# Kernel optimization log

Hardware: AMD Instinct MI355X
Metric: run time of the kernel (lower is better)

Reference implementation:

```python
import jax, jax.numpy as jnp
import numpy as np

K = 2  # kernel_size == stride, padding=0, dilation=1 -> non-overlapping 2x2x2 blocks


def setup_inputs() -> dict:
    key = jax.random.key(0)
    # (b, c, s, w, h) volumetric batch
    x = jax.random.normal(key, (8, 1, 64, 192, 192), dtype=jnp.float32)
    return {"x": x}


def _extract_blocks(x, k):
    # Faithful to extract_patches_3d with stride==kernel, padding=0, dilation=1:
    # the double unfold + permute + flat view yields rows ordered (b, c, do, ho, wo),
    # each row the flattened k*k*k patch.
    b, c, s, w, h = x.shape
    blk = x.reshape(b, c, s // k, k, w // k, k, h // k, k)
    blk = blk.transpose(0, 1, 2, 4, 6, 3, 5, 7)  # (b,c,do,ho,wo,k,k,k)
    return blk.reshape(-1, k * k * k)  # (N, k^3)


def reference(x):
    b, c, s, w, h = x.shape
    data = _extract_blocks(x, K)            # (N, 8)
    mean = jnp.mean(data, axis=0)           # (8,)
    centered = data - mean
    # torch.svd: data = U S V^T ; jax returns vh = V^T
    _, _, vh = jnp.linalg.svd(centered, full_matrices=False)
    pca_components = vh[:1].T               # (8, n_components=1)
    reduced = centered @ pca_components     # (N, 1)
    out = reduced.reshape(b, c, s // K, w // K, h // K)
    return out, mean, pca_components
```

## Files before the change

kernel.cpp:

```cpp
#include <hip/hip_runtime.h>

constexpr int NB     = 8 * 32 * 96 * 96;
constexpr int NQUAD  = NB / 4;
constexpr int NACC   = 44;
constexpr int GRID_A = 768;
constexpr int TPB    = 256;
constexpr int GRID_P = 768;

__global__ __launch_bounds__(TPB, 4)
void reduce_kernel(const float* __restrict__ x, float* __restrict__ partials) {
  float acc[NACC];
#pragma unroll
  for (int i = 0; i < NACC; ++i) acc[i] = 0.0f;

  int tid = blockIdx.x * TPB + threadIdx.x;
  const int stride = GRID_A * TPB;
  for (int q = tid; q < NQUAD; q += stride) {
    int hq = q % 24;
    int t1 = q / 24;
    int wo = t1 % 96;
    int t2 = t1 / 96;
    int so = t2 % 32;
    int b  = t2 / 32;
    const float* base = x + (((b * 64 + 2 * so) * 192 + 2 * wo) * 192 + 8 * hq);
    float4 a0 = *(const float4*)(base);
    float4 b0 = *(const float4*)(base + 4);
    float4 a1 = *(const float4*)(base + 192);
    float4 b1 = *(const float4*)(base + 196);
    float4 a2 = *(const float4*)(base + 192 * 192);
    float4 b2 = *(const float4*)(base + 192 * 192 + 4);
    float4 a3 = *(const float4*)(base + 192 * 192 + 192);
    float4 b3 = *(const float4*)(base + 192 * 192 + 196);
    float P[4][8] = {
      {a0.x, a0.y, a1.x, a1.y, a2.x, a2.y, a3.x, a3.y},
      {a0.z, a0.w, a1.z, a1.w, a2.z, a2.w, a3.z, a3.w},
      {b0.x, b0.y, b1.x, b1.y, b2.x, b2.y, b3.x, b3.y},
      {b0.z, b0.w, b1.z, b1.w, b2.z, b2.w, b3.z, b3.w}};
#pragma unroll
    for (int a = 0; a < 8; ++a)
      acc[a] += (P[0][a] + P[1][a]) + (P[2][a] + P[3][a]);
    int k = 8;
#pragma unroll
    for (int a = 0; a < 8; ++a)
#pragma unroll
      for (int c = a; c < 8; ++c) {
        float t = P[0][a] * P[0][c];
        t += P[1][a] * P[1][c];
        t += P[2][a] * P[2][c];
        t += P[3][a] * P[3][c];
        acc[k++] += t;
      }
  }

#pragma unroll
  for (int i = 0; i < NACC; ++i) {
    float v = acc[i];
    for (int off = 32; off >= 1; off >>= 1) v += __shfl_down(v, off, 64);
    acc[i] = v;
  }
  __shared__ float lds[4][NACC];
  int lane = threadIdx.x & 63;
  int wv   = threadIdx.x >> 6;
  if (lane == 0) {
#pragma unroll
    for (int i = 0; i < NACC; ++i) lds[wv][i] = acc[i];
  }
  __syncthreads();
  if (threadIdx.x < NACC) {
    float s = lds[0][threadIdx.x] + lds[1][threadIdx.x] +
              lds[2][threadIdx.x] + lds[3][threadIdx.x];
    partials[threadIdx.x * GRID_A + blockIdx.x] = s;
  }
}

__global__ __launch_bounds__(TPB)
void mid_reduce_kernel(const float* __restrict__ partials, double* __restrict__ sums_d) {
  int a = blockIdx.x;
  int t = threadIdx.x;
  const float* row = partials + a * GRID_A;
  double s = (double)row[t] + (double)row[t + 256] + (double)row[t + 512];
  for (int off = 32; off >= 1; off >>= 1) s += __shfl_down(s, off, 64);
  __shared__ double lds[4];
  if ((t & 63) == 0) lds[t >> 6] = s;
  __syncthreads();
  if (t == 0) sums_d[a] = lds[0] + lds[1] + lds[2] + lds[3];
}

__device__ __forceinline__ float rdlane(float x, int lane) {
  return __int_as_float(__builtin_amdgcn_readlane(__float_as_int(x), lane));
}

template <int P, int Q>
__device__ __forceinline__ void jrot(const float (&r)[8], float& ct, float& st) {
  float app = rdlane(r[P], P);
  float aqq = rdlane(r[Q], Q);
  float apq = rdlane(r[Q], P);
  float theta = (aqq - app) * 0.5f * __builtin_amdgcn_rcpf(apq);
  float root  = __builtin_amdgcn_sqrtf(theta * theta + 1.0f);
  float tmag  = __builtin_amdgcn_rcpf(fabsf(theta) + root);
  float tt    = copysignf(tmag, theta);
  float c     = __builtin_amdgcn_rsqf(tt * tt + 1.0f);
  float s     = tt * c;
  bool zero   = (apq == 0.0f);
  ct = zero ? 1.0f : c;
  st = zero ? 0.0f : s;
}

template <int P, int Q>
__device__ __forceinline__ void jcol(float (&r)[8], float (&v)[8], float c, float s) {
  float rp = r[P], rq = r[Q];
  r[P] = c * rp - s * rq;
  r[Q] = s * rp + c * rq;
  float vp = v[P], vq = v[Q];
  v[P] = c * vp - s * vq;
  v[Q] = s * vp + c * vq;
}

template <int P0,int Q0,int P1,int Q1,int P2,int Q2,int P3,int Q3>
__device__ __forceinline__ void jacobi_round(float (&r)[8], float (&v)[8], int i) {
  float c0,s0,c1,s1,c2,s2,c3,s3;
  jrot<P0,Q0>(r, c0, s0);
  jrot<P1,Q1>(r, c1, s1);
  jrot<P2,Q2>(r, c2, s2);
  jrot<P3,Q3>(r, c3, s3);
  jcol<P0,Q0>(r, v, c0, s0);
  jcol<P1,Q1>(r, v, c1, s1);
  jcol<P2,Q2>(r, v, c2, s2);
  jcol<P3,Q3>(r, v, c3, s3);
  float alpha = 1.0f, beta = 0.0f;
  int plane = i;
  if (i == P0) { alpha = c0; beta = -s0; plane = Q0; }
  if (i == Q0) { alpha = c0; beta =  s0; plane = P0; }
  if (i == P1) { alpha = c1; beta = -s1; plane = Q1; }
  if (i == Q1) { alpha = c1; beta =  s1; plane = P1; }
  if (i == P2) { alpha = c2; beta = -s2; plane = Q2; }
  if (i == Q2) { alpha = c2; beta =  s2; plane = P2; }
  if (i == P3) { alpha = c3; beta = -s3; plane = Q3; }
  if (i == Q3) { alpha = c3; beta =  s3; plane = P3; }
  float prow[8];
#pragma unroll
  for (int j = 0; j < 8; ++j) prow[j] = __shfl(r[j], plane, 64);
#pragma unroll
  for (int j = 0; j < 8; ++j) r[j] = alpha * r[j] + beta * prow[j];
}

__global__ __launch_bounds__(TPB, 4)
void project_solve_kernel(const float* __restrict__ x,
                          const double* __restrict__ sums_d,
                          float* __restrict__ out,
                          float* __restrict__ out_tail) {
  __shared__ double sums[NACC];
  __shared__ float s_res[9];
  int t = threadIdx.x;

  if (t < NACC) sums[t] = sums_d[t];
  __syncthreads();

  if (t < 64) {
    const int i = t & 7;
    const double invN = 1.0 / (double)NB;
    double mean[8];
#pragma unroll
    for (int j = 0; j < 8; ++j) mean[j] = sums[j] * invN;
    double mean_i = mean[0];
#pragma unroll
    for (int k = 1; k < 8; ++k) if (i == k) mean_i = mean[k];
    double rowd[8];
#pragma unroll
    for (int j = 0; j < 8; ++j) {
      int p = i < j ? i : j;
      int q = i < j ? j : i;
      int idx = 8 + p * 8 - (p * (p - 1)) / 2 + (q - p);
      rowd[j] = sums[idx] - (double)NB * mean_i * mean[j];
    }
    double tr = 0.0;
#pragma unroll
    for (int k = 0; k < 8; ++k) tr += __shfl(rowd[k], k, 64);
    double shift = tr * 0.125;

    float r[8], v[8];
#pragma unroll
    for (int j = 0; j < 8; ++j) {
      double d = rowd[j] - (j == i ? shift : 0.0);
      r[j] = (float)(d * (1.0 / 1536.0));
      v[j] = (j == i) ? 1.0f : 0.0f;
    }
#pragma unroll 1
    for (int sweep = 0; sweep < 6; ++sweep) {
      jacobi_round<7,0, 1,6, 2,5, 3,4>(r, v, i);
      jacobi_round<7,1, 2,0, 3,6, 4,5>(r, v, i);
      jacobi_round<7,2, 3,1, 4,0, 5,6>(r, v, i);
      jacobi_round<7,3, 4,2, 5,1, 6,0>(r, v, i);
      jacobi_round<7,4, 5,3, 6,2, 0,1>(r, v, i);
      jacobi_round<7,5, 6,4, 0,3, 1,2>(r, v, i);
      jacobi_round<7,6, 0,5, 1,4, 2,3>(r, v, i);
    }
    float diag[8];
#pragma unroll
    for (int k = 0; k < 8; ++k) diag[k] = rdlane(r[k], k);
    int best = 0; float bd = diag[0];
#pragma unroll
    for (int k = 1; k < 8; ++k) if (diag[k] > bd) { bd = diag[k]; best = k; }
    float vi = v[0];
#pragma unroll
    for (int k = 1; k < 8; ++k) if (best == k) vi = v[k];
    float vec[8];
#pragma unroll
    for (int k = 0; k < 8; ++k) vec[k] = rdlane(vi, k);
    float nrm2 = 0.0f;
#pragma unroll
    for (int k = 0; k < 8; ++k) nrm2 += vec[k] * vec[k];
    float inv = 1.0f / sqrtf(nrm2);
#pragma unroll
    for (int k = 0; k < 8; ++k) vec[k] *= inv;
    int m = 0; float am = fabsf(vec[0]);
#pragma unroll
    for (int k = 1; k < 8; ++k) { float aa = fabsf(vec[k]); if (aa > am) { am = aa; m = k; } }
    float vm = vec[0];
#pragma unroll
    for (int k = 1; k < 8; ++k) if (m == k) vm = vec[k];
    if (vm > 0.0f) {
#pragma unroll
      for (int k = 0; k < 8; ++k) vec[k] = -vec[k];
    }
    double c0d = 0.0;
#pragma unroll
    for (int k = 0; k < 8; ++k) c0d += mean[k] * (double)vec[k];
    float mi = (float)mean[0];
#pragma unroll
    for (int k = 1; k < 8; ++k) if (i == k) mi = (float)mean[k];
    float vl = vec[0];
#pragma unroll
    for (int k = 1; k < 8; ++k) if (i == k) vl = vec[k];

    if (t < 8) {
      s_res[t] = vl;
      if (blockIdx.x == 0) {
        out_tail[t]     = mi;
        out_tail[8 + t] = vl;
      }
    }
    if (t == 0) s_res[8] = (float)c0d;
  }
  __syncthreads();

  float w0 = s_res[0], w1 = s_res[1], w2 = s_res[2], w3 = s_res[3];
  float w4 = s_res[4], w5 = s_res[5], w6 = s_res[6], w7 = s_res[7];
  float c0 = s_res[8];
  float4* out4 = (float4*)out;
  const int stride = GRID_P * TPB;
  for (int q = blockIdx.x * TPB + t; q < NQUAD; q += stride) {
    int hq = q % 24;
    int t1 = q / 24;
    int wo = t1 % 96;
    int t2 = t1 / 96;
    int so = t2 % 32;
    int b  = t2 / 32;
    const float* base = x + (((b * 64 + 2 * so) * 192 + 2 * wo) * 192 + 8 * hq);
    float4 a0 = *(const float4*)(base);
    float4 b0 = *(const float4*)(base + 4);
    float4 a1 = *(const float4*)(base + 192);
    float4 b1 = *(const float4*)(base + 196);
    float4 a2 = *(const float4*)(base + 192 * 192);
    float4 b2 = *(const float4*)(base + 192 * 192 + 4);
    float4 a3 = *(const float4*)(base + 192 * 192 + 192);
    float4 b3 = *(const float4*)(base + 192 * 192 + 196);
    float o0 = a0.x * w0 + a0.y * w1 + a1.x * w2 + a1.y * w3
             + a2.x * w4 + a2.y * w5 + a3.x * w6 + a3.y * w7 - c0;
    float o1 = a0.z * w0 + a0.w * w1 + a1.z * w2 + a1.w * w3
             + a2.z * w4 + a2.w * w5 + a3.z * w6 + a3.w * w7 - c0;
    float o2 = b0.x * w0 + b0.y * w1 + b1.x * w2 + b1.y * w3
             + b2.x * w4 + b2.y * w5 + b3.x * w6 + b3.y * w7 - c0;
    float o3 = b0.z * w0 + b0.w * w1 + b1.z * w2 + b1.w * w3
             + b2.z * w4 + b2.w * w5 + b3.z * w6 + b3.w * w7 - c0;
    out4[q] = make_float4(o0, o1, o2, o3);
  }
}

extern "C" void kernel_launch(void* const* d_in, const int* in_sizes, int n_in,
                              void* d_out, int out_size, void* d_ws, size_t ws_size,
                              hipStream_t stream) {
  (void)in_sizes; (void)n_in; (void)out_size; (void)ws_size;
  const float* x = (const float*)d_in[0];
  float* out = (float*)d_out;
  float* partials = (float*)d_ws;
  double* sums_d  = (double*)(partials + NACC * GRID_A);

  reduce_kernel<<<GRID_A, TPB, 0, stream>>>(x, partials);
  mid_reduce_kernel<<<NACC, TPB, 0, stream>>>(partials, sums_d);
  project_solve_kernel<<<GRID_P, TPB, 0, stream>>>(x, sums_d, out, out + NB);
}
```

Baseline: 53.54 us.

## Fuse final reduction and Jacobi solve into last block of reduce kernel

Replaces the separate mid-reduce kernel with a last-block-done pattern: each block increments an atomic counter, and the final block sums all partials in double and runs the 8x8 Jacobi eigensolve once, writing the weights to a small buffer. The projection kernel then just loads nine floats instead of every block redundantly solving the eigenproblem before streaming. It also drops one Jacobi sweep (six to five). The cost is an extra memset launch, a serialized tail in a single block, and slightly less eigen-solver convergence margin.

Result: slower. 74.14 us (+38.5%).

```diff
diff --git a/kernel.cpp b/kernel.cpp
--- a/kernel.cpp
+++ b/kernel.cpp
@@ -7,13 +7,74 @@
 constexpr int TPB    = 256;
 constexpr int GRID_P = 768;
 
+__device__ __forceinline__ float rdlane(float x, int lane) {
+  return __int_as_float(__builtin_amdgcn_readlane(__float_as_int(x), lane));
+}
+
+template <int P, int Q>
+__device__ __forceinline__ void jrot(const float (&r)[8], float& ct, float& st) {
+  float app = rdlane(r[P], P);
+  float aqq = rdlane(r[Q], Q);
+  float apq = rdlane(r[Q], P);
+  float theta = (aqq - app) * 0.5f * __builtin_amdgcn_rcpf(apq);
+  float root  = __builtin_amdgcn_sqrtf(theta * theta + 1.0f);
+  float tmag  = __builtin_amdgcn_rcpf(fabsf(theta) + root);
+  float tt    = copysignf(tmag, theta);
+  float c     = __builtin_amdgcn_rsqf(tt * tt + 1.0f);
+  float s     = tt * c;
+  bool zero   = (apq == 0.0f);
+  ct = zero ? 1.0f : c;
+  st = zero ? 0.0f : s;
+}
+
+template <int P, int Q>
+__device__ __forceinline__ void jcol(float (&r)[8], float (&v)[8], float c, float s) {
+  float rp = r[P], rq = r[Q];
+  r[P] = c * rp - s * rq;
+  r[Q] = s * rp + c * rq;
+  float vp = v[P], vq = v[Q];
+  v[P] = c * vp - s * vq;
+  v[Q] = s * vp + c * vq;
+}
+
+template <int P0,int Q0,int P1,int Q1,int P2,int Q2,int P3,int Q3>
+__device__ __forceinline__ void jacobi_round(float (&r)[8], float (&v)[8], int i) {
+  float c0,s0,c1,s1,c2,s2,c3,s3;
+  jrot<P0,Q0>(r, c0, s0);
+  jrot<P1,Q1>(r, c1, s1);
+  jrot<P2,Q2>(r, c2, s2);
+  jrot<P3,Q3>(r, c3, s3);
+  jcol<P0,Q0>(r, v, c0, s0);
+  jcol<P1,Q1>(r, v, c1, s1);
+  jcol<P2,Q2>(r, v, c2, s2);
+  jcol<P3,Q3>(r, v, c3, s3);
+  float alpha = 1.0f, beta = 0.0f;
+  int plane = i;
+  if (i == P0) { alpha = c0; beta = -s0; plane = Q0; }
+  if (i == Q0) { alpha = c0; beta =  s0; plane = P0; }
+  if (i == P1) { alpha = c1; beta = -s1; plane = Q1; }
+  if (i == Q1) { alpha = c1; beta =  s1; plane = P1; }
+  if (i == P2) { alpha = c2; beta = -s2; plane = Q2; }
+  if (i == Q2) { alpha = c2; beta =  s2; plane = P2; }
+  if (i == P3) { alpha = c3; beta = -s3; plane = Q3; }
+  if (i == Q3) { alpha = c3; beta =  s3; plane = P3; }
+  float prow[8];
+#pragma unroll
+  for (int j = 0; j < 8; ++j) prow[j] = __shfl(r[j], plane, 64);
+#pragma unroll
+  for (int j = 0; j < 8; ++j) r[j] = alpha * r[j] + beta * prow[j];
+}
+
 __global__ __launch_bounds__(TPB, 4)
-void reduce_kernel(const float* __restrict__ x, float* __restrict__ partials) {
+void reduce_solve_kernel(const float* __restrict__ x, float* __restrict__ partials,
+                         unsigned int* __restrict__ ctr, float* __restrict__ res,
+                         float* __restrict__ out_tail) {
   float acc[NACC];
 #pragma unroll
   for (int i = 0; i < NACC; ++i) acc[i] = 0.0f;
 
-  int tid = blockIdx.x * TPB + threadIdx.x;
+  int t = threadIdx.x;
+  int tid = blockIdx.x * TPB + t;
   const int stride = GRID_A * TPB;
   for (int q = tid; q < NQUAD; q += stride) {
     int hq = q % 24;
@@ -44,11 +105,11 @@
     for (int a = 0; a < 8; ++a)
 #pragma unroll
       for (int c = a; c < 8; ++c) {
-        float t = P[0][a] * P[0][c];
-        t += P[1][a] * P[1][c];
-        t += P[2][a] * P[2][c];
-        t += P[3][a] * P[3][c];
-        acc[k++] += t;
+        float tt = P[0][a] * P[0][c];
+        tt += P[1][a] * P[1][c];
+        tt += P[2][a] * P[2][c];
+        tt += P[3][a] * P[3][c];
+        acc[k++] += tt;
       }
   }
 
@@ -59,191 +120,138 @@
     acc[i] = v;
   }
   __shared__ float lds[4][NACC];
-  int lane = threadIdx.x & 63;
-  int wv   = threadIdx.x >> 6;
+  int lane = t & 63;
+  int wv   = t >> 6;
   if (lane == 0) {
 #pragma unroll
     for (int i = 0; i < NACC; ++i) lds[wv][i] = acc[i];
   }
   __syncthreads();
-  if (threadIdx.x < NACC) {
-    float s = lds[0][threadIdx.x] + lds[1][threadIdx.x] +
-              lds[2][threadIdx.x] + lds[3][threadIdx.x];
-    partials[threadIdx.x * GRID_A + blockIdx.x] = s;
-  }
-}
-
-__global__ __launch_bounds__(TPB)
-void mid_reduce_kernel(const float* __restrict__ partials, double* __restrict__ sums_d) {
-  int a = blockIdx.x;
-  int t = threadIdx.x;
-  const float* row = partials + a * GRID_A;
-  double s = (double)row[t] + (double)row[t + 256] + (double)row[t + 512];
-  for (int off = 32; off >= 1; off >>= 1) s += __shfl_down(s, off, 64);
-  __shared__ double lds[4];
-  if ((t & 63) == 0) lds[t >> 6] = s;
-  __syncthreads();
-  if (t == 0) sums_d[a] = lds[0] + lds[1] + lds[2] + lds[3];
-}
-
-__device__ __forceinline__ float rdlane(float x, int lane) {
-  return __int_as_float(__builtin_amdgcn_readlane(__float_as_int(x), lane));
-}
-
-template <int P, int Q>
-__device__ __forceinline__ void jrot(const float (&r)[8], float& ct, float& st) {
-  float app = rdlane(r[P], P);
-  float aqq = rdlane(r[Q], Q);
-  float apq = rdlane(r[Q], P);
-  float theta = (aqq - app) * 0.5f * __builtin_amdgcn_rcpf(apq);
-  float root  = __builtin_amdgcn_sqrtf(theta * theta + 1.0f);
-  float tmag  = __builtin_amdgcn_rcpf(fabsf(theta) + root);
-  float tt    = copysignf(tmag, theta);
-  float c     = __builtin_amdgcn_rsqf(tt * tt + 1.0f);
-  float s     = tt * c;
-  bool zero   = (apq == 0.0f);
-  ct = zero ? 1.0f : c;
-  st = zero ? 0.0f : s;
-}
-
-template <int P, int Q>
-__device__ __forceinline__ void jcol(float (&r)[8], float (&v)[8], float c, float s) {
-  float rp = r[P], rq = r[Q];
-  r[P] = c * rp - s * rq;
-  r[Q] = s * rp + c * rq;
-  float vp = v[P], vq = v[Q];
-  v[P] = c * vp - s * vq;
-  v[Q] = s * vp + c * vq;
-}
-
-template <int P0,int Q0,int P1,int Q1,int P2,int Q2,int P3,int Q3>
-__device__ __forceinline__ void jacobi_round(float (&r)[8], float (&v)[8], int i) {
-  float c0,s0,c1,s1,c2,s2,c3,s3;
-  jrot<P0,Q0>(r, c0, s0);
-  jrot<P1,Q1>(r, c1, s1);
-  jrot<P2,Q2>(r, c2, s2);
-  jrot<P3,Q3>(r, c3, s3);
-  jcol<P0,Q0>(r, v, c0, s0);
-  jcol<P1,Q1>(r, v, c1, s1);
-  jcol<P2,Q2>(r, v, c2, s2);
-  jcol<P3,Q3>(r, v, c3, s3);
-  float alpha = 1.0f, beta = 0.0f;
-  int plane = i;
-  if (i == P0) { alpha = c0; beta = -s0; plane = Q0; }
-  if (i == Q0) { alpha = c0; beta =  s0; plane = P0; }
-  if (i == P1) { alpha = c1; beta = -s1; plane = Q1; }
-  if (i == Q1) { alpha = c1; beta =  s1; plane = P1; }
-  if (i == P2) { alpha = c2; beta = -s2; plane = Q2; }
-  if (i == Q2) { alpha = c2; beta =  s2; plane = P2; }
-  if (i == P3) { alpha = c3; beta = -s3; plane = Q3; }
-  if (i == Q3) { alpha = c3; beta =  s3; plane = P3; }
-  float prow[8];
-#pragma unroll
-  for (int j = 0; j < 8; ++j) prow[j] = __shfl(r[j], plane, 64);
-#pragma unroll
-  for (int j = 0; j < 8; ++j) r[j] = alpha * r[j] + beta * prow[j];
+  if (t < NACC) {
+    float s = lds[0][t] + lds[1][t] + lds[2][t] + lds[3][t];
+    partials[t * GRID_A + blockIdx.x] = s;
+  }
+
+  __shared__ bool is_last;
+  __syncthreads();
+  if (t == 0) {
+    __threadfence();
+    unsigned int old = atomicAdd(ctr, 1u);
+    is_last = (old == (unsigned int)(GRID_A - 1));
+  }
+  __syncthreads();
+  if (!is_last) return;
+  __threadfence();
+
+  __shared__ double pd[NACC][4];
+  __shared__ double sums[NACC];
+  if (t < NACC * 4) {
+    int a = t >> 2, qq = t & 3;
+    const float4* p = (const float4*)(partials + a * GRID_A + qq * 192);
+    double s = 0.0;
+#pragma unroll
+    for (int j = 0; j < 48; ++j) {
+      float4 u = p[j];
+      s += (double)u.x + (double)u.y + (double)u.z + (double)u.w;
+    }
+    pd[a][qq] = s;
+  }
+  __syncthreads();
+  if (t < NACC) sums[t] = pd[t][0] + pd[t][1] + pd[t][2] + pd[t][3];
+  __syncthreads();
+  if (t >= 64) return;
+
+  const int i = t & 7;
+  const double invN = 1.0 / (double)NB;
+  double mean[8];
+#pragma unroll
+  for (int j = 0; j < 8; ++j) mean[j] = sums[j] * invN;
+  double mean_i = mean[0];
+#pragma unroll
+  for (int k = 1; k < 8; ++k) if (i == k) mean_i = mean[k];
+  double rowd[8];
+#pragma unroll
+  for (int j = 0; j < 8; ++j) {
+    int p = i < j ? i : j;
+    int q = i < j ? j : i;
+    int idx = 8 + p * 8 - (p * (p - 1)) / 2 + (q - p);
+    rowd[j] = sums[idx] - (double)NB * mean_i * mean[j];
+  }
+  double tr = 0.0;
+#pragma unroll
+  for (int k = 0; k < 8; ++k) tr += __shfl(rowd[k], k, 64);
+  double shift = tr * 0.125;
+
+  float r[8], v[8];
+#pragma unroll
+  for (int j = 0; j < 8; ++j) {
+    double d = rowd[j] - (j == i ? shift : 0.0);
+    r[j] = (float)(d * (1.0 / 1536.0));
+    v[j] = (j == i) ? 1.0f : 0.0f;
+  }
+#pragma unroll 1
+  for (int sweep = 0; sweep < 5; ++sweep) {
+    jacobi_round<7,0, 1,6, 2,5, 3,4>(r, v, i);
+    jacobi_round<7,1, 2,0, 3,6, 4,5>(r, v, i);
+    jacobi_round<7,2, 3,1, 4,0, 5,6>(r, v, i);
+    jacobi_round<7,3, 4,2, 5,1, 6,0>(r, v, i);
+    jacobi_round<7,4, 5,3, 6,2, 0,1>(r, v, i);
+    jacobi_round<7,5, 6,4, 0,3, 1,2>(r, v, i);
+    jacobi_round<7,6, 0,5, 1,4, 2,3>(r, v, i);
+  }
+  float diag[8];
+#pragma unroll
+  for (int k = 0; k < 8; ++k) diag[k] = rdlane(r[k], k);
+  int best = 0; float bd = diag[0];
+#pragma unroll
+  for (int k = 1; k < 8; ++k) if (diag[k] > bd) { bd = diag[k]; best = k; }
+  float vi = v[0];
+#pragma unroll
+  for (int k = 1; k < 8; ++k) if (best == k) vi = v[k];
+  float vec[8];
+#pragma unroll
+  for (int k = 0; k < 8; ++k) vec[k] = rdlane(vi, k);
+  float nrm2 = 0.0f;
+#pragma unroll
+  for (int k = 0; k < 8; ++k) nrm2 += vec[k] * vec[k];
+  float inv = 1.0f / sqrtf(nrm2);
+#pragma unroll
+  for (int k = 0; k < 8; ++k) vec[k] *= inv;
+  int m = 0; float am = fabsf(vec[0]);
+#pragma unroll
+  for (int k = 1; k < 8; ++k) { float aa = fabsf(vec[k]); if (aa > am) { am = aa; m = k; } }
+  float vm = vec[0];
+#pragma unroll
+  for (int k = 1; k < 8; ++k) if (m == k) vm = vec[k];
+  if (vm > 0.0f) {
+#pragma unroll
+    for (int k = 0; k < 8; ++k) vec[k] = -vec[k];
+  }
+  double c0d = 0.0;
+#pragma unroll
+  for (int k = 0; k < 8; ++k) c0d += mean[k] * (double)vec[k];
+  float mi = (float)mean[0];
+#pragma unroll
+  for (int k = 1; k < 8; ++k) if (i == k) mi = (float)mean[k];
+  float vl = vec[0];
+#pragma unroll
+  for (int k = 1; k < 8; ++k) if (i == k) vl = vec[k];
+
+  if (t < 8) {
+    res[t]          = vl;
+    out_tail[t]     = mi;
+    out_tail[8 + t] = vl;
+  }
+  if (t == 0) res[8] = (float)c0d;
 }
 
 __global__ __launch_bounds__(TPB, 4)
-void project_solve_kernel(const float* __restrict__ x,
-                          const double* __restrict__ sums_d,
-                          float* __restrict__ out,
-                          float* __restrict__ out_tail) {
-  __shared__ double sums[NACC];
+void project_kernel(const float* __restrict__ x, const float* __restrict__ res,
+                    float* __restrict__ out) {
   __shared__ float s_res[9];
   int t = threadIdx.x;
-
-  if (t < NACC) sums[t] = sums_d[t];
-  __syncthreads();
-
-  if (t < 64) {
-    const int i = t & 7;
-    const double invN = 1.0 / (double)NB;
-    double mean[8];
-#pragma unroll
-    for (int j = 0; j < 8; ++j) mean[j] = sums[j] * invN;
-    double mean_i = mean[0];
-#pragma unroll
-    for (int k = 1; k < 8; ++k) if (i == k) mean_i = mean[k];
-    double rowd[8];
-#pragma unroll
-    for (int j = 0; j < 8; ++j) {
-      int p = i < j ? i : j;
-      int q = i < j ? j : i;
-      int idx = 8 + p * 8 - (p * (p - 1)) / 2 + (q - p);
-      rowd[j] = sums[idx] - (double)NB * mean_i * mean[j];
-    }
-    double tr = 0.0;
-#pragma unroll
-    for (int k = 0; k < 8; ++k) tr += __shfl(rowd[k], k, 64);
-    double shift = tr * 0.125;
-
-    float r[8], v[8];
-#pragma unroll
-    for (int j = 0; j < 8; ++j) {
-      double d = rowd[j] - (j == i ? shift : 0.0);
-      r[j] = (float)(d * (1.0 / 1536.0));
-      v[j] = (j == i) ? 1.0f : 0.0f;
-    }
-#pragma unroll 1
-    for (int sweep = 0; sweep < 6; ++sweep) {
-      jacobi_round<7,0, 1,6, 2,5, 3,4>(r, v, i);
-      jacobi_round<7,1, 2,0, 3,6, 4,5>(r, v, i);
-      jacobi_round<7,2, 3,1, 4,0, 5,6>(r, v, i);
-      jacobi_round<7,3, 4,2, 5,1, 6,0>(r, v, i);
-      jacobi_round<7,4, 5,3, 6,2, 0,1>(r, v, i);
-      jacobi_round<7,5, 6,4, 0,3, 1,2>(r, v, i);
-      jacobi_round<7,6, 0,5, 1,4, 2,3>(r, v, i);
-    }
-    float diag[8];
-#pragma unroll
-    for (int k = 0; k < 8; ++k) diag[k] = rdlane(r[k], k);
-    int best = 0; float bd = diag[0];
-#pragma unroll
-    for (int k = 1; k < 8; ++k) if (diag[k] > bd) { bd = diag[k]; best = k; }
-    float vi = v[0];
-#pragma unroll
-    for (int k = 1; k < 8; ++k) if (best == k) vi = v[k];
-    float vec[8];
-#pragma unroll
-    for (int k = 0; k < 8; ++k) vec[k] = rdlane(vi, k);
-    float nrm2 = 0.0f;
-#pragma unroll
-    for (int k = 0; k < 8; ++k) nrm2 += vec[k] * vec[k];
-    float inv = 1.0f / sqrtf(nrm2);
-#pragma unroll
-    for (int k = 0; k < 8; ++k) vec[k] *= inv;
-    int m = 0; float am = fabsf(vec[0]);
-#pragma unroll
-    for (int k = 1; k < 8; ++k) { float aa = fabsf(vec[k]); if (aa > am) { am = aa; m = k; } }
-    float vm = vec[0];
-#pragma unroll
-    for (int k = 1; k < 8; ++k) if (m == k) vm = vec[k];
-    if (vm > 0.0f) {
-#pragma unroll
-      for (int k = 0; k < 8; ++k) vec[k] = -vec[k];
-    }
-    double c0d = 0.0;
-#pragma unroll
-    for (int k = 0; k < 8; ++k) c0d += mean[k] * (double)vec[k];
-    float mi = (float)mean[0];
-#pragma unroll
-    for (int k = 1; k < 8; ++k) if (i == k) mi = (float)mean[k];
-    float vl = vec[0];
-#pragma unroll
-    for (int k = 1; k < 8; ++k) if (i == k) vl = vec[k];
-
-    if (t < 8) {
-      s_res[t] = vl;
-      if (blockIdx.x == 0) {
-        out_tail[t]     = mi;
-        out_tail[8 + t] = vl;
-      }
-    }
-    if (t == 0) s_res[8] = (float)c0d;
-  }
-  __syncthreads();
-
+  if (t < 9) s_res[t] = res[t];
+  __syncthreads();
   float w0 = s_res[0], w1 = s_res[1], w2 = s_res[2], w3 = s_res[3];
   float w4 = s_res[4], w5 = s_res[5], w6 = s_res[6], w7 = s_res[7];
   float c0 = s_res[8];
@@ -283,10 +291,11 @@
   (void)in_sizes; (void)n_in; (void)out_size; (void)ws_size;
   const float* x = (const float*)d_in[0];
   float* out = (float*)d_out;
-  float* partials = (float*)d_ws;
-  double* sums_d  = (double*)(partials + NACC * GRID_A);
-
-  reduce_kernel<<<GRID_A, TPB, 0, stream>>>(x, partials);
-  mid_reduce_kernel<<<NACC, TPB, 0, stream>>>(partials, sums_d);
-  project_solve_kernel<<<GRID_P, TPB, 0, stream>>>(x, sums_d, out, out + NB);
-}
+  float* partials   = (float*)d_ws;
+  float* res        = partials + NACC * GRID_A;
+  unsigned int* ctr = (unsigned int*)(res + 16);
+
+  hipMemsetAsync((void*)ctr, 0, sizeof(unsigned int), stream);
+  reduce_solve_kernel<<<GRID_A, TPB, 0, stream>>>(x, partials, ctr, res, out + NB);
+  project_kernel<<<GRID_P, TPB, 0, stream>>>(x, res, out);
+}
```
